# Kernel optimization log

Hardware: AMD Instinct MI355X
Metric: run time of the kernel (lower is better)

Reference implementation:

```python
import jax, jax.numpy as jnp
import numpy as np

NUM_CLASSES = 5
TEMPERATURE = 3.0
BATCH = 4_194_304


def setup_inputs() -> dict:
    key = jax.random.key(0)
    k1, k2 = jax.random.split(key)
    quality_score = jax.random.uniform(k1, (BATCH,), dtype=jnp.float32)
    class_logits = jax.random.normal(k2, (BATCH, NUM_CLASSES), dtype=jnp.float32)
    return {"quality_score": quality_score, "class_logits": class_logits}


def _soft_targets(score, num_classes):
    # Vectorized version of the per-sample python loop in the torch module.
    C = num_classes
    # int(clamp(score*C, 0, C-1)) -> floor for non-negative scores
    idx = jnp.floor(jnp.clip(score * C, 0.0, C - 1)).astype(jnp.int32)
    center = (idx.astype(score.dtype) + 0.5) / C
    dist = jnp.abs(score - center) * C
    cond_lo = (idx > 0) & (score < center)          # spill to class idx-1
    cond_hi = (idx < C - 1) & (score > center)      # spill to class idx+1
    has_nb = cond_lo | cond_hi
    main_val = jnp.where(has_nb, 1.0 - dist, 1.0)
    nb_idx = idx - cond_lo.astype(jnp.int32) + cond_hi.astype(jnp.int32)
    nb_val = jnp.where(has_nb, dist, 0.0)
    cols = jnp.arange(C)
    # [B, C] dense soft targets built by broadcasted one-hot masks (no scatter)
    soft = (main_val[:, None] * (cols[None, :] == idx[:, None])
            + nb_val[:, None] * (cols[None, :] == nb_idx[:, None]))
    return soft


def reference(quality_score, class_logits):
    T = TEMPERATURE
    C = class_logits.shape[-1]
    B = class_logits.shape[0]
    soft = _soft_targets(quality_score, C)
    p = jax.nn.softmax(soft / T, axis=-1)               # targets (probs)
    logq = jax.nn.log_softmax(class_logits / T, axis=-1)
    # F.kl_div(logq, p, reduction='batchmean') = sum p*(log p - logq) / B
    kl = jnp.sum(p * (jnp.log(p) - logq)) / B
    return kl * T * T
```

## Files before the change

kernel.cpp:

```cpp
#include <hip/hip_runtime.h>
#include <math.h>


constexpr int   kC     = 5;
constexpr float kInvT  = 1.0f / 3.0f;
constexpr float kExp13 = 1.3956124250860895f;
constexpr int   kBatch = 4194304;

constexpr int kThreads       = 256;
constexpr int kQuadsPerBlock = kThreads;
constexpr int kBlocks        = (kBatch / 4) / kQuadsPerBlock;

__device__ __forceinline__ float kl_quad(float4 P0, float4 P1, float4 P2,
                                         float4 P3, float4 P4, float4 s4) {
    const float v[20] = {P0.x, P0.y, P0.z, P0.w,
                         P1.x, P1.y, P1.z, P1.w,
                         P2.x, P2.y, P2.z, P2.w,
                         P3.x, P3.y, P3.z, P3.w,
                         P4.x, P4.y, P4.z, P4.w};
    const float ss[4] = {s4.x, s4.y, s4.z, s4.w};

    float acc = 0.0f;
    #pragma unroll
    for (int r = 0; r < 4; ++r) {
        const float s  = ss[r];
        const float l0 = v[r * 5 + 0], l1 = v[r * 5 + 1], l2 = v[r * 5 + 2],
                    l3 = v[r * 5 + 3], l4 = v[r * 5 + 4];

        const float sc     = fminf(fmaxf(s * 5.0f, 0.0f), 4.0f);
        const int   idx    = (int)sc;
        const float center = ((float)idx + 0.5f) * 0.2f;
        float       d      = fabsf(s - center) * 5.0f;
        const bool  lo     = (idx > 0) && (s < center);
        const bool  hi     = (idx < kC - 1) && (s > center);
        const bool  nb     = lo || hi;
        d = nb ? d : 0.0f;
        const int nbi = idx + (hi ? 1 : 0) - (lo ? 1 : 0);

        const float e_nb   = __expf(d * kInvT);
        const float e_main = kExp13 * __builtin_amdgcn_rcpf(e_nb);

        const float S = l0 + l1 + l2 + l3 + l4;
        const float l_main = (idx == 0) ? l0 : (idx == 1) ? l1 :
                             (idx == 2) ? l2 : (idx == 3) ? l3 : l4;
        const float l_nb   = (nbi == 0) ? l0 : (nbi == 1) ? l1 :
                             (nbi == 2) ? l2 : (nbi == 3) ? l3 : l4;

        const float Zq = __expf(l0 * kInvT) + __expf(l1 * kInvT) +
                         __expf(l2 * kInvT) + __expf(l3 * kInvT) +
                         __expf(l4 * kInvT);

        const float Zp  = e_main + e_nb + 3.0f;
        const float rZp = __builtin_amdgcn_rcpf(Zp);
        const float Spa = e_main * (1.0f - d) + e_nb * d;
        const float Spl = e_main * l_main + e_nb * l_nb + (S - l_main - l_nb);

        acc += kInvT * (Spa - Spl) * rZp + __logf(Zq * rZp);
    }
    return acc;
}

__global__ __launch_bounds__(kThreads) void kl_partial_kernel(
    const float* __restrict__ score,
    const float* __restrict__ logits,
    float* __restrict__ partial) {

    __shared__ float4 slog4[4 * 320];

    const int t    = threadIdx.x;
    const int wave = t >> 6;
    const int lane = t & 63;

    const size_t q = (size_t)blockIdx.x * kQuadsPerBlock + t;

    const float4* gsrc = reinterpret_cast<const float4*>(logits)
                       + (size_t)blockIdx.x * (kQuadsPerBlock * 5)
                       + wave * 320;
    #pragma unroll
    for (int j = 0; j < 5; ++j) {
        __builtin_amdgcn_global_load_lds(
            (const __attribute__((address_space(1))) void*)(gsrc + j * 64 + lane),
            (__attribute__((address_space(3))) void*)(&slog4[wave * 320 + j * 64]),
            16, 0, 0);
    }

    const float4 sA = reinterpret_cast<const float4*>(score)[q];

    asm volatile("s_waitcnt vmcnt(0)" ::: "memory");

    const int a0 = wave * 320 + lane * 5;
    float acc = kl_quad(slog4[a0], slog4[a0 + 1], slog4[a0 + 2],
                        slog4[a0 + 3], slog4[a0 + 4], sA);

    #pragma unroll
    for (int off = 32; off > 0; off >>= 1) acc += __shfl_down(acc, off, 64);

    __shared__ float wsum[kThreads / 64];
    if (lane == 0) wsum[wave] = acc;
    __syncthreads();
    if (t == 0) {
        float b = 0.0f;
        #pragma unroll
        for (int w = 0; w < kThreads / 64; ++w) b += wsum[w];
        partial[blockIdx.x] = b;
    }
}

__global__ __launch_bounds__(256) void kl_final_kernel(
    const float* __restrict__ partial,
    float* __restrict__ out) {
    const int t = threadIdx.x;
    const float4* p4 = reinterpret_cast<const float4*>(partial);
    const float4 a = p4[t], b = p4[t + 256], c = p4[t + 512], d = p4[t + 768];
    float acc = a.x + a.y + a.z + a.w + b.x + b.y + b.z + b.w
              + c.x + c.y + c.z + c.w + d.x + d.y + d.z + d.w;

    #pragma unroll
    for (int off = 32; off > 0; off >>= 1) acc += __shfl_down(acc, off, 64);

    __shared__ float wsum[4];
    if ((t & 63) == 0) wsum[t >> 6] = acc;
    __syncthreads();
    if (t == 0) {
        out[0] = (wsum[0] + wsum[1] + wsum[2] + wsum[3]) * (9.0f / (float)kBatch);
    }
}

extern "C" void kernel_launch(void* const* d_in, const int* in_sizes, int n_in,
                              void* d_out, int out_size, void* d_ws, size_t ws_size,
                              hipStream_t stream) {
    const float* score  = (const float*)d_in[0];
    const float* logits = (const float*)d_in[1];
    float* out     = (float*)d_out;
    float* partial = (float*)d_ws;

    kl_partial_kernel<<<kBlocks, kThreads, 0, stream>>>(score, logits, partial);
    kl_final_kernel<<<1, 256, 0, stream>>>(partial, out);
}
```

Baseline: 136.6 us.

## Double-buffer LDS staging across four tiles per block with partial vmcnt waits

Each block now processes four 256-quad tiles instead of one. It uses two LDS buffers so the global-to-LDS loads of the next tile overlap with compute on the current one, gated by s_waitcnt vmcnt(6). The grid shrinks fourfold and the final reduction reads a quarter as many partials. Fewer blocks means fewer waves in flight to hide latency, and the hand-counted vmcnt values must match the issued loads exactly, including the score load.

Measured after the change: 139.8 us. 1.02x slower.

```diff
diff --git a/kernel.cpp b/kernel.cpp
--- a/kernel.cpp
+++ b/kernel.cpp
@@ -8,8 +8,9 @@
 constexpr int   kBatch = 4194304;
 
 constexpr int kThreads       = 256;
-constexpr int kQuadsPerBlock = kThreads;
-constexpr int kBlocks        = (kBatch / 4) / kQuadsPerBlock;
+constexpr int kQuadsPerTile  = kThreads;
+constexpr int kTilesPerBlock = 4;
+constexpr int kBlocks = (kBatch / 4) / (kQuadsPerTile * kTilesPerBlock);
 
 __device__ __forceinline__ float kl_quad(float4 P0, float4 P1, float4 P2,
                                          float4 P3, float4 P4, float4 s4) {
@@ -65,44 +66,58 @@
     const float* __restrict__ logits,
     float* __restrict__ partial) {
 
-    __shared__ float4 slog4[4 * 320];
+    __shared__ float4 sbuf[2][4][320];
 
     const int t    = threadIdx.x;
     const int wave = t >> 6;
     const int lane = t & 63;
 
-    const size_t q = (size_t)blockIdx.x * kQuadsPerBlock + t;
+    const float4* __restrict__ glog = reinterpret_cast<const float4*>(logits);
+    const float4* __restrict__ gsc  = reinterpret_cast<const float4*>(score);
+    const size_t tile0 = (size_t)blockIdx.x * kTilesPerBlock;
 
-    const float4* gsrc = reinterpret_cast<const float4*>(logits)
-                       + (size_t)blockIdx.x * (kQuadsPerBlock * 5)
-                       + wave * 320;
-    #pragma unroll
-    for (int j = 0; j < 5; ++j) {
-        __builtin_amdgcn_global_load_lds(
-            (const __attribute__((address_space(1))) void*)(gsrc + j * 64 + lane),
-            (__attribute__((address_space(3))) void*)(&slog4[wave * 320 + j * 64]),
-            16, 0, 0);
-    }
+    auto stage = [&](int tt, int b) -> float4 {
+        const size_t q0 = (tile0 + tt) * kQuadsPerTile;
+        const float4* src = glog + q0 * 5 + wave * 320;
+        #pragma unroll
+        for (int j = 0; j < 5; ++j) {
+            __builtin_amdgcn_global_load_lds(
+                (const __attribute__((address_space(1))) void*)(src + j * 64 + lane),
+                (__attribute__((address_space(3))) void*)(&sbuf[b][wave][j * 64]),
+                16, 0, 0);
+        }
+        return gsc[q0 + t];
+    };
+    auto consume = [&](int b, float4 s4) -> float {
+        const int a0 = lane * 5;
+        return kl_quad(sbuf[b][wave][a0], sbuf[b][wave][a0 + 1],
+                       sbuf[b][wave][a0 + 2], sbuf[b][wave][a0 + 3],
+                       sbuf[b][wave][a0 + 4], s4);
+    };
 
-    const float4 sA = reinterpret_cast<const float4*>(score)[q];
-
+    float acc = 0.0f;
+    float4 s0 = stage(0, 0);
+    float4 s1 = stage(1, 1);
+    asm volatile("s_waitcnt vmcnt(6)" ::: "memory");
+    acc += consume(0, s0);
+    s0 = stage(2, 0);
+    asm volatile("s_waitcnt vmcnt(6)" ::: "memory");
+    acc += consume(1, s1);
+    s1 = stage(3, 1);
+    asm volatile("s_waitcnt vmcnt(6)" ::: "memory");
+    acc += consume(0, s0);
     asm volatile("s_waitcnt vmcnt(0)" ::: "memory");
-
-    const int a0 = wave * 320 + lane * 5;
-    float acc = kl_quad(slog4[a0], slog4[a0 + 1], slog4[a0 + 2],
-                        slog4[a0 + 3], slog4[a0 + 4], sA);
+    acc += consume(1, s1);
 
     #pragma unroll
     for (int off = 32; off > 0; off >>= 1) acc += __shfl_down(acc, off, 64);
 
-    __shared__ float wsum[kThreads / 64];
+    __syncthreads();
+    float* wsum = reinterpret_cast<float*>(&sbuf[0][0][0]);
     if (lane == 0) wsum[wave] = acc;
     __syncthreads();
     if (t == 0) {
-        float b = 0.0f;
-        #pragma unroll
-        for (int w = 0; w < kThreads / 64; ++w) b += wsum[w];
-        partial[blockIdx.x] = b;
+        partial[blockIdx.x] = wsum[0] + wsum[1] + wsum[2] + wsum[3];
     }
 }
 
@@ -111,9 +126,8 @@
     float* __restrict__ out) {
     const int t = threadIdx.x;
     const float4* p4 = reinterpret_cast<const float4*>(partial);
-    const float4 a = p4[t], b = p4[t + 256], c = p4[t + 512], d = p4[t + 768];
-    float acc = a.x + a.y + a.z + a.w + b.x + b.y + b.z + b.w
-              + c.x + c.y + c.z + c.w + d.x + d.y + d.z + d.w;
+    const float4 a = p4[t];
+    float acc = a.x + a.y + a.z + a.w;
 
     #pragma unroll
     for (int off = 32; off > 0; off >>= 1) acc += __shfl_down(acc, off, 64);
```
